# Optimization experiments

Hardware: AMD Instinct MI355X
Metric: run time of the kernel (lower is better)

## Reference

```python
import jax, jax.numpy as jnp
import numpy as np

N, F, H, C = 8192, 256, 256, 40
LP = 0.2  # LeakyReLU slope


def setup_inputs() -> dict:
    key = jax.random.key(0)
    ks = jax.random.split(key, 11)
    s = 1.0 / np.sqrt(F)
    return {
        "x": jax.random.normal(ks[0], (N, F), jnp.float32),
        "adj_f": jax.random.uniform(ks[1], (N, N), jnp.float32) / N,
        "adj_a": jax.random.uniform(ks[2], (N, N), jnp.float32) / N,
        "Wp": jax.random.normal(ks[3], (F, F), jnp.float32) * s,
        "bp": jax.random.normal(ks[4], (F,), jnp.float32) * s,
        "Wg": jax.random.normal(ks[5], (F, F), jnp.float32) * s,
        "Wb": jax.random.normal(ks[6], (F, F), jnp.float32) * s,
        "W1": jax.random.normal(ks[7], (F, H), jnp.float32) * s,
        "b1": jax.random.normal(ks[8], (H,), jnp.float32) * s,
        "W2": jax.random.normal(ks[9], (H, C), jnp.float32) * s,
        "b2": jax.random.normal(ks[10], (C,), jnp.float32) * s,
    }


def reference(x, adj_f, adj_a, Wp, bp, Wg, Wb, W1, b1, W2, b2):
    # --- DynamicPrompt.forward ---
    # GraphConvolution: adj_f @ (x @ Wp) + bp, then ReLU
    base_prompt = jax.nn.relu(adj_f @ (x @ Wp) + bp)  # [N, F]
    # adj_a.fill_diagonal_(0)
    idx = jnp.arange(N)
    adj_a0 = adj_a.at[idx, idx].set(0.0)
    neighbor = adj_a0 @ x                             # [N, F]
    gamma = jax.nn.leaky_relu(neighbor @ Wg, LP) + 1.0
    beta = jax.nn.leaky_relu(neighbor @ Wb, LP)
    learned_prompt = gamma * base_prompt + beta
    # F.normalize: L2 along dim=1, eps=1e-12
    nrm = jnp.linalg.norm(learned_prompt, axis=1, keepdims=True)
    learned_prompt = learned_prompt / jnp.maximum(nrm, 1e-12)
    # --- mix prompt into input, run frozen teacher GCN (eval: no dropout) ---
    x_in = 0.5 * (x + learned_prompt)
    h = jax.nn.relu(adj_a @ (x_in @ W1) + b1)         # gc1
    logits = adj_a @ (h @ W2) + b2                    # gc2
    return jax.nn.log_softmax(logits, axis=1)         # [N, C]
```

## Files before the change

kernel.cpp:

```cpp
#include <hip/hip_runtime.h>

typedef unsigned short u16;
typedef __attribute__((ext_vector_type(8))) short bf16x8;
typedef __attribute__((ext_vector_type(4))) float f32x4;

__device__ __forceinline__ u16 f2bf(float f) {
  union { float f; unsigned u; } v; v.f = f;
  unsigned r = v.u + 0x7FFFu + ((v.u >> 16) & 1u);
  return (u16)(r >> 16);
}
__device__ __forceinline__ float bf2f(u16 h) {
  union { unsigned u; float f; } v; v.u = ((unsigned)h) << 16; return v.f;
}
__device__ __forceinline__ unsigned pk2(float a, float b) {
  return (unsigned)f2bf(a) | ((unsigned)f2bf(b) << 16);
}
__device__ __forceinline__ unsigned cvtpk(float a, float b) {
  unsigned r;
  asm("v_cvt_pk_bf16_f32 %0, %1, %2" : "=v"(r) : "v"(a), "v"(b));
  return r;
}
__device__ __forceinline__ void gld16(const void* g, void* l) {
  __builtin_amdgcn_global_load_lds(
      (const __attribute__((address_space(1))) unsigned int*)g,
      (__attribute__((address_space(3))) unsigned int*)l, 16, 0, 0);
}

__global__ __launch_bounds__(256)
void prep_w_k(const float* __restrict__ Wp, const float* __restrict__ Wg,
              const float* __restrict__ Wb, const float* __restrict__ W1,
              const float* __restrict__ W2, u16* __restrict__ WpT,
              u16* __restrict__ WgbT, u16* __restrict__ W1T,
              u16* __restrict__ W2T) {
  int z = blockIdx.z;
  const float* in; u16* out; int C = 256;
  if (z == 0) { in = Wp; out = WpT; }
  else if (z == 1) { in = Wg; out = WgbT; }
  else if (z == 2) { in = Wb; out = WgbT + 65536; }
  else if (z == 3) { in = W1; out = W1T; }
  else { in = W2; out = W2T; C = 40; if (blockIdx.x >= 2) return; }
  __shared__ float tile[32][33];
  int tj = blockIdx.x * 32, ti = blockIdx.y * 32;
  int t = threadIdx.x, c = t & 31, r0 = t >> 5;
#pragma unroll
  for (int p = 0; p < 4; ++p) {
    int r = r0 + p * 8;
    tile[r][c] = (tj + c < C) ? in[(size_t)(ti + r) * C + (tj + c)] : 0.f;
  }
  __syncthreads();
#pragma unroll
  for (int p = 0; p < 4; ++p) {
    int rr = r0 + p * 8;
    out[(size_t)(tj + rr) * 256 + (ti + c)] = f2bf(tile[c][rr]);
  }
}

__global__ __launch_bounds__(256)
void prep_x_k(const float* __restrict__ x, u16* __restrict__ xT,
              u16* __restrict__ xbf) {
  __shared__ float tile[32][33];
  int tj = blockIdx.x * 32, ti = blockIdx.y * 32;
  int t = threadIdx.x, c = t & 31, r0 = t >> 5;
#pragma unroll
  for (int p = 0; p < 4; ++p) {
    int r = r0 + p * 8;
    float v = x[(size_t)(ti + r) * 256 + (tj + c)];
    tile[r][c] = v;
    xbf[(size_t)(ti + r) * 256 + (tj + c)] = f2bf(v);
  }
  __syncthreads();
#pragma unroll
  for (int p = 0; p < 4; ++p) {
    int rr = r0 + p * 8;
    xT[(size_t)(tj + rr) * 8192 + (ti + c)] = f2bf(tile[c][rr]);
  }
}

__global__ __launch_bounds__(256)
void diag_k(const float* __restrict__ adj, float* __restrict__ d) {
  int i = blockIdx.x * 256 + threadIdx.x;
  d[i] = bf2f(f2bf(adj[(size_t)i * 8193]));
}

template <int BN, bool ABF, bool WRB, bool PACK>
__global__ __launch_bounds__(512, 1)
void bgemm_k(const void* __restrict__ Av, const u16* __restrict__ Bt,
             void* __restrict__ part, u16* __restrict__ Aout) {
  constexpr int BM = 128;
  constexpr int KP = 1024;
  constexpr int NSTEP = KP / 64;
  constexpr int MT = 8192 / BM;
  constexpr int AROWB = ABF ? 128 : 256;
  constexpr int ABYTES = BM * AROWB;
  constexpr int NA = ABYTES / 8192;
  constexpr int NB = BN * 128 / 8192;
  constexpr int FR = 2;
  constexpr int FC = BN / 32;

  __shared__ char sA[2][ABYTES];
  __shared__ u16 sB[2][BN * 64];
  const int t = threadIdx.x, lane = t & 63, w = t >> 6;
  const int l15 = lane & 15, lhi = lane >> 4;
  const int s = ((blockIdx.x & 7) << 6) | (blockIdx.x >> 3);
  const int kp = s >> 6, m = s & (MT - 1);
  const int mBase = m * BM;
  const int kpBase = kp * KP;
  const int waveM = (w >> 1) * 32;
  const int waveN = (w & 1) * (BN / 2);

  f32x4 acc[FR][FC];
#pragma unroll
  for (int a = 0; a < FR; ++a)
#pragma unroll
    for (int b = 0; b < FC; ++b) acc[a][b] = (f32x4){0.f, 0.f, 0.f, 0.f};

  auto stage = [&](int buf, int tt) {
    const int k0 = kpBase + tt * 64;
#pragma unroll
    for (int i = 0; i < NA; ++i) {
      int L = i * 8192 + t * 16;
      int row, kb;
      if (ABF) { row = L >> 7; kb = (L & 127) ^ ((row & 7) << 4); }
      else     { row = L >> 8; kb = (L & 255) ^ ((row & 7) << 4); }
      const char* g;
      if (ABF)
        g = (const char*)Av + (((size_t)(mBase + row)) << 14) + ((size_t)k0 << 1) + kb;
      else
        g = (const char*)Av + (((size_t)(mBase + row)) << 15) + ((size_t)k0 << 2) + kb;
      gld16(g, (char*)sA[buf] + L);
    }
#pragma unroll
    for (int i = 0; i < NB; ++i) {
      int L = i * 8192 + t * 16;
      int n = L >> 7;
      int kb = (L & 127) ^ ((n & 7) << 4);
      gld16((const char*)Bt + ((size_t)n << 14) + ((size_t)k0 << 1) + kb,
            (char*)sB[buf] + L);
    }
  };

  stage(0, 0);
  asm volatile("s_waitcnt vmcnt(0)" ::: "memory");
  __builtin_amdgcn_s_barrier();

  for (int st = 0; st < NSTEP; ++st) {
    const int cur = st & 1;
    if (st + 1 < NSTEP) stage(cur ^ 1, st + 1);
    const char* sa = (const char*)sA[cur];
    const char* sb = (const char*)sB[cur];
    if (WRB && !ABF) {
      const int k0 = kpBase + st * 64;
      int r = t >> 2, cb = (t & 3) << 6;
      int sw = (r & 7) << 4;
      const char* sar = sa + r * 256;
      f32x4 v0 = *(const f32x4*)(sar + ((cb) ^ sw));
      f32x4 v1 = *(const f32x4*)(sar + ((cb + 16) ^ sw));
      f32x4 v2 = *(const f32x4*)(sar + ((cb + 32) ^ sw));
      f32x4 v3 = *(const f32x4*)(sar + ((cb + 48) ^ sw));
      uint4 q0, q1;
      q0.x = cvtpk(v0.x, v0.y); q0.y = cvtpk(v0.z, v0.w);
      q0.z = cvtpk(v1.x, v1.y); q0.w = cvtpk(v1.z, v1.w);
      q1.x = cvtpk(v2.x, v2.y); q1.y = cvtpk(v2.z, v2.w);
      q1.z = cvtpk(v3.x, v3.y); q1.w = cvtpk(v3.z, v3.w);
      u16* dst = Aout + ((size_t)(mBase + r) << 13) + k0 + (cb >> 2);
      *(uint4*)dst = q0;
      *(uint4*)(dst + 8) = q1;
    }
#pragma unroll
    for (int ks = 0; ks < 2; ++ks) {
      bf16x8 av[FR], bv[FC];
#pragma unroll
      for (int fr = 0; fr < FR; ++fr) {
        int row = waveM + fr * 16 + l15;
        if (ABF) {
          int off = row * 128 + ((ks * 64 + lhi * 16) ^ ((row & 7) << 4));
          av[fr] = *(const bf16x8*)(sa + off);
        } else {
          int inrow = ks * 128 + lhi * 32;
          int sw = (row & 7) << 4;
          const char* sar = sa + row * 256;
          f32x4 x0 = *(const f32x4*)(sar + (inrow ^ sw));
          f32x4 x1 = *(const f32x4*)(sar + ((inrow + 16) ^ sw));
          union { bf16x8 v; unsigned u[4]; } p;
          p.u[0] = cvtpk(x0.x, x0.y); p.u[1] = cvtpk(x0.z, x0.w);
          p.u[2] = cvtpk(x1.x, x1.y); p.u[3] = cvtpk(x1.z, x1.w);
          av[fr] = p.v;
        }
      }
#pragma unroll
      for (int fc = 0; fc < FC; ++fc) {
        int n = waveN + fc * 16 + l15;
        int off = n * 128 + ((ks * 64 + lhi * 16) ^ ((n & 7) << 4));
        bv[fc] = *(const bf16x8*)(sb + off);
      }
#pragma unroll
      for (int fr = 0; fr < FR; ++fr)
#pragma unroll
        for (int fc = 0; fc < FC; ++fc)
          acc[fr][fc] = __builtin_amdgcn_mfma_f32_16x16x32_bf16(
              av[fr], bv[fc], acc[fr][fc], 0, 0, 0);
    }
    asm volatile("s_waitcnt vmcnt(0)" ::: "memory");
    __builtin_amdgcn_s_barrier();
  }

  if (PACK) {
    unsigned* pp = (unsigned*)part + (size_t)kp * 8192 * 128 + (size_t)mBase * 128;
#pragma unroll
    for (int fr = 0; fr < FR; ++fr)
#pragma unroll
      for (int fcp = 0; fcp < FC / 2; ++fcp) {
        int g = (waveN >> 5) + fcp;
        int r0 = waveM + fr * 16 + lhi * 4;
#pragma unroll
        for (int j = 0; j < 4; ++j)
          pp[(size_t)(r0 + j) * 128 + g * 16 + l15] =
              cvtpk(acc[fr][2 * fcp][j], acc[fr][2 * fcp + 1][j]);
      }
  } else {
    float* pp = (float*)part + (size_t)kp * 8192 * BN + (size_t)mBase * BN;
#pragma unroll
    for (int fr = 0; fr < FR; ++fr)
#pragma unroll
      for (int fc = 0; fc < FC; ++fc) {
        int col = waveN + fc * 16 + l15;
        int r0 = waveM + fr * 16 + lhi * 4;
#pragma unroll
        for (int j = 0; j < 4; ++j)
          pp[(size_t)(r0 + j) * BN + col] = acc[fr][fc][j];
      }
  }
}

template <int BN, int EPI, int OMODE>
__global__ __launch_bounds__(256)
void sgemm_k(const u16* __restrict__ Abf, const u16* __restrict__ Bt,
             float* __restrict__ C, int ldc, u16* __restrict__ Ct) {
  __shared__ u16 sA[32 * 256];
  __shared__ u16 sB[BN * 256];
  const int t = threadIdx.x, lane = t & 63, w = t >> 6;
  const int rowBase = blockIdx.x * 32;
  const u16* bt = Bt + (size_t)blockIdx.y * BN * 256;
  const int colBlk = blockIdx.y * BN;

#pragma unroll
  for (int i = 0; i < 4; ++i) {
    int lin = ((w * 4 + i) << 10) + (lane << 4);
    int row = lin >> 9;
    int kb = (lin & 511) ^ ((row & 7) << 4);
    const char* g = (const char*)Abf + ((size_t)(rowBase + row) << 9) + kb;
    gld16(g, (char*)sA + ((w * 4 + i) << 10));
  }
#pragma unroll
  for (int i = 0; i < BN / 8; ++i) {
    int lin = ((w * (BN / 8) + i) << 10) + (lane << 4);
    int n = lin >> 9;
    int kb = (lin & 511) ^ ((n & 7) << 4);
    const char* g = (const char*)bt + ((size_t)n << 9) + kb;
    gld16(g, (char*)sB + ((w * (BN / 8) + i) << 10));
  }
  __syncthreads();

  constexpr int FC = BN / 32;
  const int waveM = (w & 1) * 16;
  const int waveN = (w >> 1) * (BN / 2);
  f32x4 acc[FC];
#pragma unroll
  for (int b = 0; b < FC; ++b) acc[b] = (f32x4){0.f, 0.f, 0.f, 0.f};

#pragma unroll
  for (int ks = 0; ks < 8; ++ks) {
    int row = waveM + (lane & 15);
    int offA = (row * 512 + ks * 64 + ((lane >> 4) * 16)) ^ ((row & 7) << 4);
    bf16x8 av = *(const bf16x8*)((const char*)sA + offA);
#pragma unroll
    for (int fc = 0; fc < FC; ++fc) {
      int n = waveN + fc * 16 + (lane & 15);
      int offB = (n * 512 + ks * 64 + ((lane >> 4) * 16)) ^ ((n & 7) << 4);
      bf16x8 bv = *(const bf16x8*)((const char*)sB + offB);
      acc[fc] = __builtin_amdgcn_mfma_f32_16x16x32_bf16(av, bv, acc[fc], 0, 0, 0);
    }
  }

#pragma unroll
  for (int fc = 0; fc < FC; ++fc) {
    int col = waveN + fc * 16 + (lane & 15);
    int r0 = rowBase + waveM + ((lane >> 4) << 2);
    float o[4];
#pragma unroll
    for (int j = 0; j < 4; ++j) {
      float xv = acc[fc][j];
      if (EPI == 1) xv = fmaxf(xv, 0.f);
      if (EPI == 2) xv = (xv > 0.f) ? xv : 0.2f * xv;
      o[j] = xv;
    }
    if (OMODE == 1) {
      uint2 q; q.x = pk2(o[0], o[1]); q.y = pk2(o[2], o[3]);
      *(uint2*)(Ct + (size_t)(colBlk + col) * 8192 + r0) = q;
    } else if (OMODE == 2) {
#pragma unroll
      for (int j = 0; j < 4; ++j)
        Ct[(size_t)(r0 + j) * ldc + colBlk + col] = f2bf(o[j]);
    } else {
#pragma unroll
      for (int j = 0; j < 4; ++j)
        C[(size_t)(r0 + j) * ldc + colBlk + col] = o[j];
    }
  }
}

template <int MODE>
__global__ __launch_bounds__(256)
void reduce8p_k(const unsigned* __restrict__ part, const float* __restrict__ bias,
                const float* __restrict__ dd, const u16* __restrict__ xbf,
                u16* __restrict__ Cb) {
  const int tid = threadIdx.x;
  const int row = blockIdx.x * 2 + (tid >> 7);
  const int uc = tid & 127;
  const size_t S = (size_t)8192 * 128;
  const size_t b = (size_t)row * 128 + uc;
  float slo = 0.f, shi = 0.f;
#pragma unroll
  for (int p = 0; p < 8; ++p) {
    unsigned v = part[b + (size_t)p * S];
    slo += bf2f((u16)(v & 0xffff));
    shi += bf2f((u16)(v >> 16));
  }
  const int clo = (uc & 15) + ((uc >> 4) << 5), chi = clo + 16;
  if (MODE == 1) {
    float d = dd[row];
    slo -= d * bf2f(xbf[(size_t)row * 256 + clo]);
    shi -= d * bf2f(xbf[(size_t)row * 256 + chi]);
  } else {
    slo = fmaxf(slo + bias[clo], 0.f);
    shi = fmaxf(shi + bias[chi], 0.f);
  }
  Cb[(size_t)row * 256 + clo] = f2bf(slo);
  Cb[(size_t)row * 256 + chi] = f2bf(shi);
}

__global__ __launch_bounds__(128)
void fuse_red_k(const unsigned* __restrict__ part, const float* __restrict__ bp,
                const u16* __restrict__ gbuf, const u16* __restrict__ xbf,
                u16* __restrict__ xin_bf) {
  const int row = blockIdx.x, uc = threadIdx.x;
  const size_t S = (size_t)8192 * 128;
  const size_t b = (size_t)row * 128 + uc;
  float slo = 0.f, shi = 0.f;
#pragma unroll
  for (int p = 0; p < 8; ++p) {
    unsigned v = part[b + (size_t)p * S];
    slo += bf2f((u16)(v & 0xffff));
    shi += bf2f((u16)(v >> 16));
  }
  const int clo = (uc & 15) + ((uc >> 4) << 5), chi = clo + 16;
  float baselo = fmaxf(slo + bp[clo], 0.f);
  float basehi = fmaxf(shi + bp[chi], 0.f);
  float glo = bf2f(gbuf[(size_t)row * 512 + clo]);
  float ghi = bf2f(gbuf[(size_t)row * 512 + chi]);
  float btlo = bf2f(gbuf[(size_t)row * 512 + 256 + clo]);
  float bthi = bf2f(gbuf[(size_t)row * 512 + 256 + chi]);
  float lplo = (glo + 1.f) * baselo + btlo;
  float lphi = (ghi + 1.f) * basehi + bthi;
  float ss = lplo * lplo + lphi * lphi;
#pragma unroll
  for (int off = 32; off >= 1; off >>= 1) ss += __shfl_xor(ss, off);
  __shared__ float wsum[2];
  if ((uc & 63) == 0) wsum[uc >> 6] = ss;
  __syncthreads();
  float inv = 1.f / fmaxf(sqrtf(wsum[0] + wsum[1]), 1e-12f);
  xin_bf[(size_t)row * 256 + clo] =
      f2bf(0.5f * (bf2f(xbf[(size_t)row * 256 + clo]) + lplo * inv));
  xin_bf[(size_t)row * 256 + chi] =
      f2bf(0.5f * (bf2f(xbf[(size_t)row * 256 + chi]) + lphi * inv));
}

__global__ __launch_bounds__(256)
void reduce_lsm_k(const float* __restrict__ part, const float* __restrict__ b2,
                  float* __restrict__ out) {
  const int t = threadIdx.x, lane = t & 63, w = t >> 6;
  const int row = blockIdx.x * 4 + w;
  const size_t i = (size_t)row * 64 + lane;
  const size_t S = (size_t)8192 * 64;
  float v = 0.f;
#pragma unroll
  for (int p = 0; p < 8; ++p) v += part[i + (size_t)p * S];
  v = (lane < 40) ? v + b2[lane] : -1e30f;
  float mx = v;
#pragma unroll
  for (int off = 32; off >= 1; off >>= 1) mx = fmaxf(mx, __shfl_xor(mx, off));
  float e = (lane < 40) ? expf(v - mx) : 0.f;
#pragma unroll
  for (int off = 32; off >= 1; off >>= 1) e += __shfl_xor(e, off);
  float ls = mx + logf(e);
  if (lane < 40) out[(size_t)row * 40 + lane] = v - ls;
}

extern "C" void kernel_launch(void* const* d_in, const int* in_sizes, int n_in,
                              void* d_out, int out_size, void* d_ws, size_t ws_size,
                              hipStream_t stream) {
  const float* x = (const float*)d_in[0];
  const float* adj_f = (const float*)d_in[1];
  const float* adj_a = (const float*)d_in[2];
  const float* Wp = (const float*)d_in[3];
  const float* bp = (const float*)d_in[4];
  const float* Wg = (const float*)d_in[5];
  const float* Wb = (const float*)d_in[6];
  const float* W1 = (const float*)d_in[7];
  const float* b1 = (const float*)d_in[8];
  const float* W2 = (const float*)d_in[9];
  const float* b2 = (const float*)d_in[10];
  float* out = (float*)d_out;

  char* ws = (char*)d_ws;
  size_t off = 0;
  auto alloc = [&](size_t bytes) {
    char* p = ws + off;
    off += (bytes + 255) & ~(size_t)255;
    return p;
  };
  unsigned* partU = (unsigned*)alloc((size_t)8 * 8192 * 128 * 4);
  float* partF = (float*)partU;
  u16* featT = (u16*)alloc((size_t)256 * 8192 * 2);
  u16* featT64 = (u16*)alloc((size_t)64 * 8192 * 2);
  u16* xT = (u16*)alloc((size_t)256 * 8192 * 2);
  u16* xbf = (u16*)alloc((size_t)8192 * 256 * 2);
  u16* xin_bf = (u16*)alloc((size_t)8192 * 256 * 2);
  u16* neigh_bf = (u16*)alloc((size_t)8192 * 256 * 2);
  u16* h_bf = (u16*)alloc((size_t)8192 * 256 * 2);
  u16* gbuf = (u16*)alloc((size_t)8192 * 512 * 2);
  u16* WpT = (u16*)alloc(256 * 256 * 2);
  u16* WgbT = (u16*)alloc(512 * 256 * 2);
  u16* W1T = (u16*)alloc(256 * 256 * 2);
  u16* W2T = (u16*)alloc(64 * 256 * 2);
  float* dd = (float*)alloc(8192 * 4);

  const size_t adjBytes = (size_t)8192 * 8192 * 2;
  bool useBf = (ws_size >= off + adjBytes + 256);
  u16* adj_bf = useBf ? (u16*)alloc(adjBytes) : nullptr;

  dim3 b256(256), b512(512);
  prep_w_k<<<dim3(8, 8, 5), b256, 0, stream>>>(Wp, Wg, Wb, W1, W2, WpT, WgbT, W1T, W2T);
  prep_x_k<<<dim3(8, 256), b256, 0, stream>>>(x, xT, xbf);
  diag_k<<<32, b256, 0, stream>>>(adj_a, dd);

  if (useBf)
    bgemm_k<256, false, true, true><<<512, b512, 0, stream>>>(adj_a, xT, partU, adj_bf);
  else
    bgemm_k<256, false, false, true><<<512, b512, 0, stream>>>(adj_a, xT, partU, nullptr);
  reduce8p_k<1><<<4096, b256, 0, stream>>>(partU, nullptr, dd, xbf, neigh_bf);
  sgemm_k<128, 2, 2><<<dim3(256, 4), b256, 0, stream>>>(neigh_bf, WgbT, nullptr, 512, gbuf);
  sgemm_k<128, 0, 1><<<dim3(256, 2), b256, 0, stream>>>(xbf, WpT, nullptr, 0, featT);
  bgemm_k<256, false, false, true><<<512, b512, 0, stream>>>(adj_f, featT, partU, nullptr);
  fuse_red_k<<<8192, dim3(128), 0, stream>>>(partU, bp, gbuf, xbf, xin_bf);
  sgemm_k<128, 0, 1><<<dim3(256, 2), b256, 0, stream>>>(xin_bf, W1T, nullptr, 0, featT);
  if (useBf)
    bgemm_k<256, true, false, true><<<512, b512, 0, stream>>>(adj_bf, featT, partU, nullptr);
  else
    bgemm_k<256, false, false, true><<<512, b512, 0, stream>>>(adj_a, featT, partU, nullptr);
  reduce8p_k<2><<<4096, b256, 0, stream>>>(partU, b1, nullptr, nullptr, h_bf);
  sgemm_k<64, 0, 1><<<dim3(256, 1), b256, 0, stream>>>(h_bf, W2T, nullptr, 0, featT64);
  if (useBf)
    bgemm_k<64, true, false, false><<<512, b512, 0, stream>>>(adj_bf, featT64, partU, nullptr);
  else
    bgemm_k<64, false, false, false><<<512, b512, 0, stream>>>(adj_a, featT64, partU, nullptr);
  reduce_lsm_k<<<2048, b256, 0, stream>>>(partF, b2, out);
}
```

Before: 364.7 us.

## Restructure adjacency GEMM into 3-stage async pipeline with smaller tiles and fewer K-splits

The big adjacency GEMM kernel moves from 512-thread blocks with BM=128 and 8 K-partitions to 256-thread blocks with BM=64 and 4 K-partitions of 2048. It uses a triple-buffered LDS ring with counted vmcnt waits instead of full drains. This lets loads for the next stages stay in flight during the MFMA compute and halves the split-K partial traffic the reduction kernels read. The trade-off is more loop iterations per block, fewer waves per block, and counted waits that must match the number of outstanding loads, including the extra stores on the write-back path.

```diff
diff --git a/kernel.cpp b/kernel.cpp
--- a/kernel.cpp
+++ b/kernel.cpp
@@ -24,6 +24,10 @@
   __builtin_amdgcn_global_load_lds(
       (const __attribute__((address_space(1))) unsigned int*)g,
       (__attribute__((address_space(3))) unsigned int*)l, 16, 0, 0);
+}
+template <int N>
+__device__ __forceinline__ void waitvm() {
+  asm volatile("s_waitcnt vmcnt(%0)" ::"n"(N) : "memory");
 }
 
 __global__ __launch_bounds__(256)
@@ -83,26 +87,28 @@
 }
 
 template <int BN, bool ABF, bool WRB, bool PACK>
-__global__ __launch_bounds__(512, 1)
+__global__ __launch_bounds__(256, ((BN == 64 && ABF) ? 3 : 1))
 void bgemm_k(const void* __restrict__ Av, const u16* __restrict__ Bt,
              void* __restrict__ part, u16* __restrict__ Aout) {
-  constexpr int BM = 128;
-  constexpr int KP = 1024;
+  constexpr int BM = 64;
+  constexpr int KP = 2048;
   constexpr int NSTEP = KP / 64;
   constexpr int MT = 8192 / BM;
   constexpr int AROWB = ABF ? 128 : 256;
   constexpr int ABYTES = BM * AROWB;
-  constexpr int NA = ABYTES / 8192;
-  constexpr int NB = BN * 128 / 8192;
+  constexpr int NA = ABYTES / 4096;
+  constexpr int NB = BN * 128 / 4096;
+  constexpr int LS = NA + NB;
+  constexpr int ST = WRB ? 2 : 0;
   constexpr int FR = 2;
   constexpr int FC = BN / 32;
 
-  __shared__ char sA[2][ABYTES];
-  __shared__ u16 sB[2][BN * 64];
+  __shared__ char sA[3][ABYTES];
+  __shared__ u16 sB[3][BN * 64];
   const int t = threadIdx.x, lane = t & 63, w = t >> 6;
   const int l15 = lane & 15, lhi = lane >> 4;
   const int s = ((blockIdx.x & 7) << 6) | (blockIdx.x >> 3);
-  const int kp = s >> 6, m = s & (MT - 1);
+  const int kp = s >> 7, m = s & (MT - 1);
   const int mBase = m * BM;
   const int kpBase = kp * KP;
   const int waveM = (w >> 1) * 32;
@@ -118,7 +124,7 @@
     const int k0 = kpBase + tt * 64;
 #pragma unroll
     for (int i = 0; i < NA; ++i) {
-      int L = i * 8192 + t * 16;
+      int L = i * 4096 + t * 16;
       int row, kb;
       if (ABF) { row = L >> 7; kb = (L & 127) ^ ((row & 7) << 4); }
       else     { row = L >> 8; kb = (L & 255) ^ ((row & 7) << 4); }
@@ -131,7 +137,7 @@
     }
 #pragma unroll
     for (int i = 0; i < NB; ++i) {
-      int L = i * 8192 + t * 16;
+      int L = i * 4096 + t * 16;
       int n = L >> 7;
       int kb = (L & 127) ^ ((n & 7) << 4);
       gld16((const char*)Bt + ((size_t)n << 14) + ((size_t)k0 << 1) + kb,
@@ -140,12 +146,19 @@
   };
 
   stage(0, 0);
-  asm volatile("s_waitcnt vmcnt(0)" ::: "memory");
-  __builtin_amdgcn_s_barrier();
-
+  stage(1, 1);
+  stage(2, 2);
+
+  int cur = 0;
   for (int st = 0; st < NSTEP; ++st) {
-    const int cur = st & 1;
-    if (st + 1 < NSTEP) stage(cur ^ 1, st + 1);
+    if (st == 0) waitvm<2 * LS>();
+    else if (st == 1) waitvm<2 * LS + ST>();
+    else if (st < NSTEP - 2) waitvm<2 * LS + 2 * ST>();
+    else if (st == NSTEP - 2) waitvm<LS + 2 * ST>();
+    else waitvm<2 * ST>();
+    __builtin_amdgcn_s_barrier();
+    __builtin_amdgcn_sched_barrier(0);
+
     const char* sa = (const char*)sA[cur];
     const char* sb = (const char*)sB[cur];
     if (WRB && !ABF) {
@@ -200,8 +213,10 @@
           acc[fr][fc] = __builtin_amdgcn_mfma_f32_16x16x32_bf16(
               av[fr], bv[fc], acc[fr][fc], 0, 0, 0);
     }
-    asm volatile("s_waitcnt vmcnt(0)" ::: "memory");
+    __builtin_amdgcn_sched_barrier(0);
     __builtin_amdgcn_s_barrier();
+    if (st + 3 < NSTEP) stage(cur, st + 3);
+    cur = (cur == 2) ? 0 : cur + 1;
   }
 
   if (PACK) {
@@ -311,7 +326,7 @@
 
 template <int MODE>
 __global__ __launch_bounds__(256)
-void reduce8p_k(const unsigned* __restrict__ part, const float* __restrict__ bias,
+void reduce4p_k(const unsigned* __restrict__ part, const float* __restrict__ bias,
                 const float* __restrict__ dd, const u16* __restrict__ xbf,
                 u16* __restrict__ Cb) {
   const int tid = threadIdx.x;
@@ -321,7 +336,7 @@
   const size_t b = (size_t)row * 128 + uc;
   float slo = 0.f, shi = 0.f;
 #pragma unroll
-  for (int p = 0; p < 8; ++p) {
+  for (int p = 0; p < 4; ++p) {
     unsigned v = part[b + (size_t)p * S];
     slo += bf2f((u16)(v & 0xffff));
     shi += bf2f((u16)(v >> 16));
@@ -348,7 +363,7 @@
   const size_t b = (size_t)row * 128 + uc;
   float slo = 0.f, shi = 0.f;
 #pragma unroll
-  for (int p = 0; p < 8; ++p) {
+  for (int p = 0; p < 4; ++p) {
     unsigned v = part[b + (size_t)p * S];
     slo += bf2f((u16)(v & 0xffff));
     shi += bf2f((u16)(v >> 16));
@@ -384,7 +399,7 @@
   const size_t S = (size_t)8192 * 64;
   float v = 0.f;
 #pragma unroll
-  for (int p = 0; p < 8; ++p) v += part[i + (size_t)p * S];
+  for (int p = 0; p < 4; ++p) v += part[i + (size_t)p * S];
   v = (lane < 40) ? v + b2[lane] : -1e30f;
   float mx = v;
 #pragma unroll
@@ -419,7 +434,7 @@
     off += (bytes + 255) & ~(size_t)255;
     return p;
   };
-  unsigned* partU = (unsigned*)alloc((size_t)8 * 8192 * 128 * 4);
+  unsigned* partU = (unsigned*)alloc((size_t)4 * 8192 * 128 * 4);
   float* partF = (float*)partU;
   u16* featT = (u16*)alloc((size_t)256 * 8192 * 2);
   u16* featT64 = (u16*)alloc((size_t)64 * 8192 * 2);
@@ -439,30 +454,30 @@
   bool useBf = (ws_size >= off + adjBytes + 256);
   u16* adj_bf = useBf ? (u16*)alloc(adjBytes) : nullptr;
 
-  dim3 b256(256), b512(512);
+  dim3 b256(256);
   prep_w_k<<<dim3(8, 8, 5), b256, 0, stream>>>(Wp, Wg, Wb, W1, W2, WpT, WgbT, W1T, W2T);
   prep_x_k<<<dim3(8, 256), b256, 0, stream>>>(x, xT, xbf);
   diag_k<<<32, b256, 0, stream>>>(adj_a, dd);
 
   if (useBf)
-    bgemm_k<256, false, true, true><<<512, b512, 0, stream>>>(adj_a, xT, partU, adj_bf);
+    bgemm_k<256, false, true, true><<<512, b256, 0, stream>>>(adj_a, xT, partU, adj_bf);
   else
-    bgemm_k<256, false, false, true><<<512, b512, 0, stream>>>(adj_a, xT, partU, nullptr);
-  reduce8p_k<1><<<4096, b256, 0, stream>>>(partU, nullptr, dd, xbf, neigh_bf);
+    bgemm_k<256, false, false, true><<<512, b256, 0, stream>>>(adj_a, xT, partU, nullptr);
+  reduce4p_k<1><<<4096, b256, 0, stream>>>(partU, nullptr, dd, xbf, neigh_bf);
   sgemm_k<128, 2, 2><<<dim3(256, 4), b256, 0, stream>>>(neigh_bf, WgbT, nullptr, 512, gbuf);
   sgemm_k<128, 0, 1><<<dim3(256, 2), b256, 0, stream>>>(xbf, WpT, nullptr, 0, featT);
-  bgemm_k<256, false, false, true><<<512, b512, 0, stream>>>(adj_f, featT, partU, nullptr);
+  bgemm_k<256, false, false, true><<<512, b256, 0, stream>>>(adj_f, featT, partU, nullptr);
   fuse_red_k<<<8192, dim3(128), 0, stream>>>(partU, bp, gbuf, xbf, xin_bf);
   sgemm_k<128, 0, 1><<<dim3(256, 2), b256, 0, stream>>>(xin_bf, W1T, nullptr, 0, featT);
   if (useBf)
-    bgemm_k<256, true, false, true><<<512, b512, 0, stream>>>(adj_bf, featT, partU, nullptr);
+    bgemm_k<256, true, false, true><<<512, b256, 0, stream>>>(adj_bf, featT, partU, nullptr);
   else
-    bgemm_k<256, false, false, true><<<512, b512, 0, stream>>>(adj_a, featT, partU, nullptr);
-  reduce8p_k<2><<<4096, b256, 0, stream>>>(partU, b1, nullptr, nullptr, h_bf);
+    bgemm_k<256, false, false, true><<<512, b256, 0, stream>>>(adj_a, featT, partU, nullptr);
+  reduce4p_k<2><<<4096, b256, 0, stream>>>(partU, b1, nullptr, nullptr, h_bf);
   sgemm_k<64, 0, 1><<<dim3(256, 1), b256, 0, stream>>>(h_bf, W2T, nullptr, 0, featT64);
   if (useBf)
-    bgemm_k<64, true, false, false><<<512, b512, 0, stream>>>(adj_bf, featT64, partU, nullptr);
+    bgemm_k<64, true, false, false><<<512, b256, 0, stream>>>(adj_bf, featT64, partU, nullptr);
   else
-    bgemm_k<64, false, false, false><<<512, b512, 0, stream>>>(adj_a, featT64, partU, nullptr);
+    bgemm_k<64, false, false, false><<<512, b256, 0, stream>>>(adj_a, featT64, partU, nullptr);
   reduce_lsm_k<<<2048, b256, 0, stream>>>(partF, b2, out);
 }
```

New measurement: 395.3 us. +8.4%, slower.
